# Optimization experiments

Measured on AMD Instinct MI355X. Metric: run time of the kernel, lower is better.

Reference implementation:

```python
import jax, jax.numpy as jnp
import numpy as np

B, T, D = 8, 1024, 768
H, DH = 12, 64
E, K, DFF = 16, 2, 3072
EPS = 1e-5


def _ln(x, w, b):
    m = x.mean(-1, keepdims=True)
    v = ((x - m) ** 2).mean(-1, keepdims=True)
    return (x - m) * jax.lax.rsqrt(v + EPS) * w + b


def setup_inputs() -> dict:
    key = jax.random.key(0)
    ks = jax.random.split(key, 12)
    s = 0.02
    return {
        "x": jax.random.normal(ks[0], (B, T, D), jnp.float32),
        "ln1_w": jnp.ones((D,), jnp.float32),
        "ln1_b": jnp.zeros((D,), jnp.float32),
        "qkv_w": jax.random.normal(ks[1], (D, 3 * D), jnp.float32) * s,
        "qkv_b": jnp.zeros((3 * D,), jnp.float32),
        "proj_w": jax.random.normal(ks[2], (D, D), jnp.float32) * s,
        "proj_b": jnp.zeros((D,), jnp.float32),
        "ln2_w": jnp.ones((D,), jnp.float32),
        "ln2_b": jnp.zeros((D,), jnp.float32),
        "router_w": jax.random.normal(ks[3], (D, E), jnp.float32) * s,
        "w1": jax.random.normal(ks[4], (E, D, DFF), jnp.float32) * s,
        "b1": jnp.zeros((E, DFF), jnp.float32),
        "w2": jax.random.normal(ks[5], (E, DFF, D), jnp.float32) * s,
        "b2": jnp.zeros((E, D), jnp.float32),
    }


def _block(x, ln1_w, ln1_b, qkv_w, qkv_b, proj_w, proj_b,
           ln2_w, ln2_b, router_w, w1, b1, w2, b2):
    # --- attention ---
    h = _ln(x, ln1_w, ln1_b)
    qkv = h @ qkv_w + qkv_b                      # [B,T,3D]
    q, k, v = jnp.split(qkv, 3, axis=-1)
    q = q.reshape(B, T, H, DH).transpose(0, 2, 1, 3)
    k = k.reshape(B, T, H, DH).transpose(0, 2, 1, 3)
    v = v.reshape(B, T, H, DH).transpose(0, 2, 1, 3)
    scores = jnp.einsum("bhqd,bhkd->bhqk", q, k) / np.sqrt(DH)
    causal = jnp.tril(jnp.ones((T, T), bool))
    scores = jnp.where(causal, scores, -jnp.inf)
    attn = jax.nn.softmax(scores, axis=-1)
    y = jnp.einsum("bhqk,bhkd->bhqd", attn, v)
    y = y.transpose(0, 2, 1, 3).reshape(B, T, D)
    x = x + y @ proj_w + proj_b                  # residual 1

    # --- MoE FFN (dense all-experts, gated combine) ---
    z = _ln(x, ln2_w, ln2_b)                     # [B,T,D]
    probs = jax.nn.softmax(z @ router_w, axis=-1)  # [B,T,E]
    top_p, ix = jax.lax.top_k(probs, K)
    gate = (jax.nn.one_hot(ix, E, dtype=probs.dtype) * top_p[..., None]).sum(-2)  # [B,T,E]
    gate_e = jnp.moveaxis(gate, -1, 0)           # [E,B,T]

    def body(acc, ew):
        g, W1, B1, W2, B2 = ew
        out = jax.nn.gelu(z @ W1 + B1, approximate=False) @ W2 + B2
        return acc + g[..., None] * out, None

    yff, _ = jax.lax.scan(body, jnp.zeros_like(z), (gate_e, w1, b1, w2, b2))
    # MoELayer returns z + yff; Block adds x again (faithful double residual)
    return x + z + yff


def reference(x, ln1_w, ln1_b, qkv_w, qkv_b, proj_w, proj_b,
              ln2_w, ln2_b, router_w, w1, b1, w2, b2):
    return _block(x, ln1_w, ln1_b, qkv_w, qkv_b, proj_w, proj_b,
                  ln2_w, ln2_b, router_w, w1, b1, w2, b2)
```

## Files before the change

### kernel.cpp

```cpp
#include <hip/hip_runtime.h>
#include <math.h>

#define D_MODEL 768
#define T_SEQ   1024
#define B_BATCH 8
#define NTOK    8192
#define H_HEADS 12
#define DHEAD   64
#define NEXP    16
#define DFF     3072
#define NPAIR   16384
#define MAXT128 144
#define MAXT256 80

typedef unsigned short u16;
typedef unsigned int   u32;

typedef __attribute__((ext_vector_type(8))) short bf16x8;
typedef __attribute__((ext_vector_type(4))) float f32x4;
typedef __attribute__((ext_vector_type(4))) u32   u32x4;

__device__ __forceinline__ float bf2f(u16 u) { return __uint_as_float(((u32)u) << 16); }
__device__ __forceinline__ u16 f2bf(float f) {
    u32 u = __float_as_uint(f);
    return (u16)((u + 0x7FFFu + ((u >> 16) & 1u)) >> 16);
}

__device__ __forceinline__ float fast_gelu(float v) {
    float u2 = -1.5957691216f * v * (1.0f + 0.044715f * v * v);
    return v / (1.0f + __expf(u2));
}

__device__ __forceinline__ void gload16(const void* g, void* l) {
    __builtin_amdgcn_global_load_lds((const __attribute__((address_space(1))) void*)g,
                                     (__attribute__((address_space(3))) void*)l, 16, 0, 0);
}

__global__ __launch_bounds__(256) void ln_kernel(const float* __restrict__ x,
                                                 const float* __restrict__ w,
                                                 const float* __restrict__ b,
                                                 u16* __restrict__ out_bf,
                                                 float* __restrict__ out_f) {
    const int row = blockIdx.x;
    const int tid = threadIdx.x;
    const float* xr = x + (size_t)row * D_MODEL;
    float v0 = xr[tid], v1 = xr[tid + 256], v2 = xr[tid + 512];
    float s = v0 + v1 + v2;
    float s2 = v0 * v0 + v1 * v1 + v2 * v2;
#pragma unroll
    for (int o = 32; o > 0; o >>= 1) { s += __shfl_down(s, o); s2 += __shfl_down(s2, o); }
    __shared__ float red[8];
    __shared__ float stats[2];
    const int wid = tid >> 6;
    if ((tid & 63) == 0) { red[wid] = s; red[4 + wid] = s2; }
    __syncthreads();
    if (tid == 0) {
        float ts = red[0] + red[1] + red[2] + red[3];
        float ts2 = red[4] + red[5] + red[6] + red[7];
        float mean = ts * (1.0f / D_MODEL);
        float var = ts2 * (1.0f / D_MODEL) - mean * mean;
        stats[0] = mean;
        stats[1] = rsqrtf(var + 1e-5f);
    }
    __syncthreads();
    const float mean = stats[0], rstd = stats[1];
    u16* orow = out_bf + (size_t)row * D_MODEL;
    float r0 = (v0 - mean) * rstd * w[tid]       + b[tid];
    float r1 = (v1 - mean) * rstd * w[tid + 256] + b[tid + 256];
    float r2 = (v2 - mean) * rstd * w[tid + 512] + b[tid + 512];
    orow[tid] = f2bf(r0); orow[tid + 256] = f2bf(r1); orow[tid + 512] = f2bf(r2);
    if (out_f) {
        float* frow = out_f + (size_t)row * D_MODEL;
        frow[tid] = r0; frow[tid + 256] = r1; frow[tid + 512] = r2;
    }
}

__global__ __launch_bounds__(256) void transpose_cvt(const float* __restrict__ src,
                                                     u16* __restrict__ dst,
                                                     int R, int C) {
    const size_t plane = (size_t)R * C;
    src += (size_t)blockIdx.z * plane;
    dst += (size_t)blockIdx.z * plane;
    __shared__ __align__(16) u16 tile[64][72];
    const int t = threadIdx.x;
    const int r0 = blockIdx.y * 64, c0 = blockIdx.x * 64;
    {
        const int lr = t >> 2, lc = (t & 3) * 16;
        const float* sp = src + (size_t)(r0 + lr) * C + c0 + lc;
        u16 tmp[16];
#pragma unroll
        for (int j = 0; j < 4; ++j) {
            f32x4 f = *(const f32x4*)(sp + j * 4);
            tmp[j * 4 + 0] = f2bf(f[0]); tmp[j * 4 + 1] = f2bf(f[1]);
            tmp[j * 4 + 2] = f2bf(f[2]); tmp[j * 4 + 3] = f2bf(f[3]);
        }
        *(u32x4*)&tile[lr][lc]     = *(const u32x4*)&tmp[0];
        *(u32x4*)&tile[lr][lc + 8] = *(const u32x4*)&tmp[8];
    }
    __syncthreads();
    {
        const int ln = t >> 2, lk0 = (t & 3) * 16;
        u16 o[16];
#pragma unroll
        for (int j = 0; j < 16; ++j) o[j] = tile[lk0 + j][ln];
        u16* d = dst + (size_t)(c0 + ln) * R + r0 + lk0;
        *(u32x4*)&d[0] = *(const u32x4*)&o[0];
        *(u32x4*)&d[8] = *(const u32x4*)&o[8];
    }
}

template <int MODE>
__global__ __launch_bounds__(512, 2) void gemm2ph(
    const u16* __restrict__ A, const u16* __restrict__ Bt,
    const float* __restrict__ bias, void* __restrict__ Cout,
    const int* __restrict__ bucket_tok, const int* __restrict__ offsets,
    const int* __restrict__ counts, const int* __restrict__ desc_e,
    const int* __restrict__ desc_r, const int* __restrict__ tile_cnt,
    int K, int N)
{
    const u32 nwg  = gridDim.x * gridDim.y;
    const u32 orig = blockIdx.x + gridDim.x * blockIdx.y;
    const u32 flat = (nwg & 7u) ? orig : ((orig & 7u) * (nwg >> 3) + (orig >> 3));
    const int bx = (int)(flat % gridDim.x);
    const int by = (int)(flat / gridDim.x);

    int e = 0, r0 = 0, off = 0, ne = 0, row0 = 0;
    const int col0 = bx * 256;
    if constexpr (MODE >= 2) {
        if (by >= *tile_cnt) return;
        e = desc_e[by];
        r0 = desc_r[by];
        off = offsets[e];
        ne = counts[e];
    } else {
        row0 = by * 256;
    }
    if constexpr (MODE == 2) Bt += (size_t)e * D_MODEL * DFF;
    if constexpr (MODE == 3) Bt += (size_t)e * DFF * D_MODEL;

    __shared__ __align__(16) u16 As[2][256 * 64];
    __shared__ __align__(16) u16 Bs[2][256 * 64];

    const int tid = threadIdx.x;
    const int lane = tid & 63;
    const int w = tid >> 6;
    const int wm = w >> 2, wn = w & 3;
    const int fr = lane & 15, fg = lane >> 4;

    const int koff = ((((tid & 7) * 16) ^ (((tid >> 3) & 7) << 4)) >> 1);

    u32 aoff[4], boff[4];
#pragma unroll
    for (int i = 0; i < 4; ++i) {
        const int r = i * 64 + (tid >> 3);
        u32 row;
        if constexpr (MODE == 2) {
            int rb = r0 + r;
            row = (u32)bucket_tok[off + (rb < ne ? rb : 0)];
        } else if constexpr (MODE == 3) {
            int rb = r0 + r;
            row = (u32)(off + (rb < ne ? rb : (ne - 1)));
        } else {
            row = (u32)(row0 + r);
        }
        aoff[i] = row * (u32)K + (u32)koff;
        boff[i] = (u32)(col0 + r) * (u32)K + (u32)koff;
    }

    f32x4 acc[8][4] = {};
    const int nt = K >> 6;

#pragma unroll
    for (int i = 0; i < 4; ++i) gload16(A + aoff[i],  &As[0][(i * 512 + w * 64) * 8]);
#pragma unroll
    for (int i = 0; i < 4; ++i) gload16(Bt + boff[i], &Bs[0][(i * 512 + w * 64) * 8]);
    __syncthreads();

    int cur = 0;
    for (int t = 0; t < nt; ++t) {
        if (t + 1 < nt) {
            const int k0n = (t + 1) * 64;
            const int nxt = cur ^ 1;
#pragma unroll
            for (int i = 0; i < 4; ++i) gload16(A + aoff[i] + k0n,  &As[nxt][(i * 512 + w * 64) * 8]);
#pragma unroll
            for (int i = 0; i < 4; ++i) gload16(Bt + boff[i] + k0n, &Bs[nxt][(i * 512 + w * 64) * 8]);
        }
#pragma unroll
        for (int kk = 0; kk < 2; ++kk) {
            const int sw = ((kk * 64 + fg * 16) ^ ((fr & 7) << 4)) >> 1;
            bf16x8 a[8], b[4];
#pragma unroll
            for (int mi = 0; mi < 8; ++mi)
                a[mi] = *(const bf16x8*)&As[cur][(wm * 128 + mi * 16 + fr) * 64 + sw];
#pragma unroll
            for (int ni = 0; ni < 4; ++ni)
                b[ni] = *(const bf16x8*)&Bs[cur][(wn * 64 + ni * 16 + fr) * 64 + sw];
#pragma unroll
            for (int mi = 0; mi < 8; ++mi)
#pragma unroll
                for (int ni = 0; ni < 4; ++ni)
                    acc[mi][ni] = __builtin_amdgcn_mfma_f32_16x16x32_bf16(a[mi], b[ni], acc[mi][ni], 0, 0, 0);
        }
        if (t + 1 < nt) {
            __syncthreads();
            cur ^= 1;
        }
    }

    __syncthreads();
    float* slab = (float*)&As[0][0] + w * 1088;
    const int er = lane >> 2;
    const int ec = (lane & 3) * 16;
    const int colb = col0 + wn * 64 + ec;

#pragma unroll
    for (int mi = 0; mi < 8; ++mi) {
#pragma unroll
        for (int ni = 0; ni < 4; ++ni)
#pragma unroll
            for (int i = 0; i < 4; ++i)
                slab[(fg * 4 + i) * 68 + ni * 16 + fr] = acc[mi][ni][i];
        __syncthreads();
        f32x4 v[4];
#pragma unroll
        for (int q = 0; q < 4; ++q) v[q] = *(const f32x4*)&slab[er * 68 + ec + q * 4];
        const int lrow = wm * 128 + mi * 16 + er;

        if constexpr (MODE == 0) {
            u16 o[16];
#pragma unroll
            for (int q = 0; q < 4; ++q) {
                f32x4 b4 = *(const f32x4*)&bias[colb + q * 4];
#pragma unroll
                for (int j = 0; j < 4; ++j) o[q * 4 + j] = f2bf(v[q][j] + b4[j]);
            }
            u16* cp = (u16*)Cout + (size_t)(row0 + lrow) * N + colb;
            *(u32x4*)cp       = *(const u32x4*)&o[0];
            *(u32x4*)(cp + 8) = *(const u32x4*)&o[8];
        } else if constexpr (MODE == 2) {
            const int rb = r0 + lrow;
            if (rb < ne) {
                u16 o[16];
#pragma unroll
                for (int q = 0; q < 4; ++q) {
                    f32x4 b4 = *(const f32x4*)&bias[(size_t)e * DFF + colb + q * 4];
#pragma unroll
                    for (int j = 0; j < 4; ++j) o[q * 4 + j] = f2bf(fast_gelu(v[q][j] + b4[j]));
                }
                u16* cp = (u16*)Cout + (size_t)(off + rb) * N + colb;
                *(u32x4*)cp       = *(const u32x4*)&o[0];
                *(u32x4*)(cp + 8) = *(const u32x4*)&o[8];
            }
        } else {
            const int rb = r0 + lrow;
            if (rb < ne) {
                float* cp = (float*)Cout + (size_t)(off + rb) * N + colb;
#pragma unroll
                for (int q = 0; q < 4; ++q) {
                    f32x4 b4 = *(const f32x4*)&bias[(size_t)e * D_MODEL + colb + q * 4];
                    f32x4 o4;
#pragma unroll
                    for (int j = 0; j < 4; ++j) o4[j] = v[q][j] + b4[j];
                    *(f32x4*)(cp + q * 4) = o4;
                }
            }
        }
        if (mi < 7) __syncthreads();
    }
}

template <int MODE>
__global__ __launch_bounds__(512, 4) void gemm256(
    const u16* __restrict__ A, const u16* __restrict__ Bt,
    const float* __restrict__ bias, void* __restrict__ Cout,
    const float* __restrict__ resid,
    int K, int N)
{
    const u32 nwg  = gridDim.x * gridDim.y;
    const u32 orig = blockIdx.x + gridDim.x * blockIdx.y;
    const u32 flat = (nwg & 7u) ? orig : ((orig & 7u) * (nwg >> 3) + (orig >> 3));
    const int bx = (int)(flat % gridDim.x);
    const int by = (int)(flat / gridDim.x);

    const int col0 = bx * 128;
    const int row0 = by * 256;

    __shared__ __align__(16) u16 AsBs[256 * 64 + 128 * 64];
    u16* As = AsBs;
    u16* Bs = AsBs + 256 * 64;

    const int tid = threadIdx.x;
    const int lane = tid & 63;
    const int w = tid >> 6;
    const int wm = w >> 1, wn = w & 1;
    const int fr = lane & 15, fg = lane >> 4;

    const int koff = ((((tid & 7) * 16) ^ (((tid >> 3) & 7) << 4)) >> 1);

    u32 aoff[4];
#pragma unroll
    for (int i = 0; i < 4; ++i)
        aoff[i] = (u32)(row0 + i * 64 + (tid >> 3)) * (u32)K + (u32)koff;
    u32 boff[2];
#pragma unroll
    for (int i = 0; i < 2; ++i)
        boff[i] = (u32)(col0 + i * 64 + (tid >> 3)) * (u32)K + (u32)koff;

    f32x4 acc[4][4] = {};

    for (int k0 = 0; k0 < K; k0 += 64) {
        __syncthreads();
#pragma unroll
        for (int i = 0; i < 4; ++i)
            gload16(A + aoff[i] + k0, &As[(i * 512 + w * 64) * 8]);
#pragma unroll
        for (int i = 0; i < 2; ++i)
            gload16(Bt + boff[i] + k0, &Bs[(i * 512 + w * 64) * 8]);
        __syncthreads();
#pragma unroll
        for (int kk = 0; kk < 2; ++kk) {
            const int sw = ((kk * 64 + fg * 16) ^ ((fr & 7) << 4)) >> 1;
            bf16x8 a[4], b[4];
#pragma unroll
            for (int mi = 0; mi < 4; ++mi)
                a[mi] = *(const bf16x8*)&As[(wm * 64 + mi * 16 + fr) * 64 + sw];
#pragma unroll
            for (int ni = 0; ni < 4; ++ni)
                b[ni] = *(const bf16x8*)&Bs[(wn * 64 + ni * 16 + fr) * 64 + sw];
#pragma unroll
            for (int mi = 0; mi < 4; ++mi)
#pragma unroll
                for (int ni = 0; ni < 4; ++ni)
                    acc[mi][ni] = __builtin_amdgcn_mfma_f32_16x16x32_bf16(a[mi], b[ni], acc[mi][ni], 0, 0, 0);
        }
    }

    __syncthreads();
    float* slab = (float*)AsBs + w * 1088;
    const int er = lane >> 2;
    const int ec = (lane & 3) * 16;
    const int colb = col0 + wn * 64 + ec;

#pragma unroll
    for (int mi = 0; mi < 4; ++mi) {
#pragma unroll
        for (int ni = 0; ni < 4; ++ni)
#pragma unroll
            for (int i = 0; i < 4; ++i)
                slab[(fg * 4 + i) * 68 + ni * 16 + fr] = acc[mi][ni][i];
        __syncthreads();
        f32x4 v[4];
#pragma unroll
        for (int q = 0; q < 4; ++q) v[q] = *(const f32x4*)&slab[er * 68 + ec + q * 4];
        const int lrow = wm * 64 + mi * 16 + er;

        float* cp = (float*)Cout + (size_t)(row0 + lrow) * N + colb;
        const float* rp = resid + (size_t)(row0 + lrow) * N + colb;
#pragma unroll
        for (int q = 0; q < 4; ++q) {
            f32x4 b4 = *(const f32x4*)&bias[colb + q * 4];
            f32x4 r4 = *(const f32x4*)(rp + q * 4);
            f32x4 o4;
#pragma unroll
            for (int j = 0; j < 4; ++j) o4[j] = v[q][j] + b4[j] + r4[j];
            *(f32x4*)(cp + q * 4) = o4;
        }
        if (mi < 3) __syncthreads();
    }
}

template <int MODE>
__global__ __launch_bounds__(256) void gemm128f(
    const u16* __restrict__ A, const float* __restrict__ Bf,
    const float* __restrict__ bias, void* __restrict__ Cout,
    const float* __restrict__ resid,
    const int* __restrict__ bucket_tok, const int* __restrict__ offsets,
    const int* __restrict__ counts, const int* __restrict__ desc_e,
    const int* __restrict__ desc_r, const int* __restrict__ tile_cnt,
    int K, int N)
{
    int e = 0, r0 = 0, off = 0, ne = 0, row0 = 0;
    const int col0 = blockIdx.x * 128;
    if constexpr (MODE >= 2) {
        if ((int)blockIdx.y >= *tile_cnt) return;
        e = desc_e[blockIdx.y]; r0 = desc_r[blockIdx.y];
        off = offsets[e]; ne = counts[e];
    } else row0 = blockIdx.y * 128;
    if constexpr (MODE == 2) Bf += (size_t)e * D_MODEL * DFF;
    if constexpr (MODE == 3) Bf += (size_t)e * DFF * D_MODEL;

    __shared__ __align__(16) u16 AsL[128 * 32];
    __shared__ __align__(16) u16 BsL[128 * 32];

    const int tid = threadIdx.x;
    const int lane = tid & 63;
    const int w = tid >> 6;
    const int wr = (w >> 1) * 64, wc = (w & 1) * 64;
    const int fr = lane & 15, fg = lane >> 4;
    const int lrow = lane >> 2, lk = (lane & 3) * 8;

    const u16* ag[2];
#pragma unroll
    for (int i = 0; i < 2; ++i) {
        int r = i * 64 + w * 16 + lrow;
        size_t srow;
        if constexpr (MODE == 2) {
            int rb = r0 + r;
            int tok = bucket_tok[off + (rb < ne ? rb : 0)];
            srow = (size_t)tok * K;
        } else if constexpr (MODE == 3) {
            int rb = r0 + r;
            int pp = off + (rb < ne ? rb : (ne - 1));
            srow = (size_t)pp * K;
        } else srow = (size_t)(row0 + r) * K;
        ag[i] = A + srow + lk;
    }

    f32x4 acc[4][4] = {};
    for (int k0 = 0; k0 < K; k0 += 32) {
        __syncthreads();
        gload16(ag[0] + k0, &AsL[0 * 2048 + w * 512]);
        gload16(ag[1] + k0, &AsL[1 * 2048 + w * 512]);
#pragma unroll
        for (int i = 0; i < 4; ++i) {
            int s = tid + 256 * i;
            int kk = s >> 5, n4 = (s & 31) * 4;
            f32x4 f = *(const f32x4*)(Bf + (size_t)(k0 + kk) * N + col0 + n4);
            BsL[(n4 + 0) * 32 + kk] = f2bf(f[0]);
            BsL[(n4 + 1) * 32 + kk] = f2bf(f[1]);
            BsL[(n4 + 2) * 32 + kk] = f2bf(f[2]);
            BsL[(n4 + 3) * 32 + kk] = f2bf(f[3]);
        }
        __syncthreads();
        bf16x8 a[4], b[4];
#pragma unroll
        for (int mi = 0; mi < 4; ++mi)
            a[mi] = *(const bf16x8*)&AsL[(wr + mi * 16 + fr) * 32 + fg * 8];
#pragma unroll
        for (int ni = 0; ni < 4; ++ni)
            b[ni] = *(const bf16x8*)&BsL[(wc + ni * 16 + fr) * 32 + fg * 8];
#pragma unroll
        for (int mi = 0; mi < 4; ++mi)
#pragma unroll
            for (int ni = 0; ni < 4; ++ni)
                acc[mi][ni] = __builtin_amdgcn_mfma_f32_16x16x32_bf16(a[mi], b[ni], acc[mi][ni], 0, 0, 0);
    }
#pragma unroll
    for (int mi = 0; mi < 4; ++mi) {
#pragma unroll
        for (int ni = 0; ni < 4; ++ni) {
            const int lr = wr + mi * 16 + fg * 4;
            const int col = col0 + wc + ni * 16 + fr;
#pragma unroll
            for (int i = 0; i < 4; ++i) {
                float v = acc[mi][ni][i];
                if constexpr (MODE == 0) {
                    int grow = row0 + lr + i;
                    ((u16*)Cout)[(size_t)grow * N + col] = f2bf(v + bias[col]);
                } else if constexpr (MODE == 1) {
                    int grow = row0 + lr + i;
                    size_t idx = (size_t)grow * N + col;
                    ((float*)Cout)[idx] = resid[idx] + v + bias[col];
                } else if constexpr (MODE == 2) {
                    int rb = r0 + lr + i;
                    if (rb < ne) {
                        float vb = v + bias[(size_t)e * DFF + col];
                        ((u16*)Cout)[(size_t)(off + rb) * N + col] = f2bf(fast_gelu(vb));
                    }
                } else {
                    int rb = r0 + lr + i;
                    if (rb < ne) {
                        ((float*)Cout)[(size_t)(off + rb) * N + col] = v + bias[(size_t)e * D_MODEL + col];
                    }
                }
            }
        }
    }
}

__global__ __launch_bounds__(256) void attn_mfma(const u16* __restrict__ qkv,
                                                 u16* __restrict__ y) {
    const int bh = blockIdx.x;
    const int b = bh / H_HEADS, h = bh % H_HEADS;
    const int qt = gridDim.y - 1 - blockIdx.y;
    const int tid = threadIdx.x, lane = tid & 63, w = tid >> 6;
    const int fr = lane & 15, fg = lane >> 4;

    __shared__ __align__(16) u16 Ks[128][72];
    __shared__ __align__(16) u16 Vt[64][136];
    __shared__ __align__(16) u16 Ps[4][32][136];

    const int tb = b * T_SEQ + qt * 128;
    const int wrow = w * 32;

    bf16x8 aq[2][2];
#pragma unroll
    for (int rg = 0; rg < 2; ++rg) {
        const u16* qp = qkv + (size_t)(tb + wrow + rg * 16 + fr) * (3 * D_MODEL) + h * DHEAD + fg * 8;
        aq[rg][0] = *(const bf16x8*)qp;
        aq[rg][1] = *(const bf16x8*)(qp + 32);
    }
    f32x4 accO[2][4] = {};
    float m_[2][4], l_[2][4];
#pragma unroll
    for (int rg = 0; rg < 2; ++rg)
#pragma unroll
        for (int i = 0; i < 4; ++i) { m_[rg][i] = -1e30f; l_[rg][i] = 0.0f; }

    for (int kt = 0; kt <= qt; ++kt) {
        __syncthreads();
        {
#pragma unroll
            for (int it = 0; it < 2; ++it) {
                const int krow = (tid >> 2) + it * 64;
                const int c16 = (tid & 3) * 16;
                const u16* kp = qkv + (size_t)(b * T_SEQ + kt * 128 + krow) * (3 * D_MODEL)
                              + D_MODEL + h * DHEAD + c16;
                *(u32x4*)&Ks[krow][c16]     = *(const u32x4*)kp;
                *(u32x4*)&Ks[krow][c16 + 8] = *(const u32x4*)(kp + 8);
                const u16* vp = kp + D_MODEL;
                u16 vv[16];
                *(u32x4*)&vv[0] = *(const u32x4*)vp;
                *(u32x4*)&vv[8] = *(const u32x4*)(vp + 8);
#pragma unroll
                for (int j = 0; j < 16; ++j) Vt[c16 + j][krow] = vv[j];
            }
        }
        __syncthreads();

        const bool diag = (kt == qt);

#pragma unroll
        for (int rg = 0; rg < 2; ++rg) {
            f32x4 s4[8] = {};
#pragma unroll
            for (int kk = 0; kk < 2; ++kk) {
#pragma unroll
                for (int ni = 0; ni < 8; ++ni) {
                    bf16x8 bk = *(const bf16x8*)&Ks[ni * 16 + fr][kk * 32 + fg * 8];
                    s4[ni] = __builtin_amdgcn_mfma_f32_16x16x32_bf16(aq[rg][kk], bk, s4[ni], 0, 0, 0);
                }
            }
            float p[8][4];
#pragma unroll
            for (int i = 0; i < 4; ++i) {
                const int grow = qt * 128 + wrow + rg * 16 + fg * 4 + i;
                float rmax = -1e30f;
                if (!diag) {
#pragma unroll
                    for (int ni = 0; ni < 8; ++ni) {
                        float v = s4[ni][i] * 0.125f;
                        p[ni][i] = v;
                        rmax = fmaxf(rmax, v);
                    }
                } else {
#pragma unroll
                    for (int ni = 0; ni < 8; ++ni) {
                        float v = s4[ni][i] * 0.125f;
                        if (kt * 128 + ni * 16 + fr > grow) v = -1e30f;
                        p[ni][i] = v;
                        rmax = fmaxf(rmax, v);
                    }
                }
#pragma unroll
                for (int msk = 1; msk < 16; msk <<= 1) rmax = fmaxf(rmax, __shfl_xor(rmax, msk));
                const float mn = fmaxf(m_[rg][i], rmax);
                float sum = 0.0f;
#pragma unroll
                for (int ni = 0; ni < 8; ++ni) {
                    float ev = __expf(p[ni][i] - mn);
                    p[ni][i] = ev;
                    sum += ev;
                }
#pragma unroll
                for (int msk = 1; msk < 16; msk <<= 1) sum += __shfl_xor(sum, msk);
                const float sc = __expf(m_[rg][i] - mn);
                l_[rg][i] = l_[rg][i] * sc + sum;
                m_[rg][i] = mn;
#pragma unroll
                for (int ni = 0; ni < 4; ++ni) accO[rg][ni][i] *= sc;
#pragma unroll
                for (int ni = 0; ni < 8; ++ni)
                    Ps[w][rg * 16 + fg * 4 + i][ni * 16 + fr] = f2bf(p[ni][i]);
            }
        }

#pragma unroll
        for (int rg = 0; rg < 2; ++rg) {
#pragma unroll
            for (int kk = 0; kk < 4; ++kk) {
                bf16x8 ap = *(const bf16x8*)&Ps[w][rg * 16 + fr][kk * 32 + fg * 8];
#pragma unroll
                for (int ni = 0; ni < 4; ++ni) {
                    bf16x8 bv = *(const bf16x8*)&Vt[ni * 16 + fr][kk * 32 + fg * 8];
                    accO[rg][ni] = __builtin_amdgcn_mfma_f32_16x16x32_bf16(ap, bv, accO[rg][ni], 0, 0, 0);
                }
            }
        }
    }

#pragma unroll
    for (int rg = 0; rg < 2; ++rg) {
#pragma unroll
        for (int i = 0; i < 4; ++i) {
            const float inv = 1.0f / l_[rg][i];
            u16* yp = y + (size_t)(tb + wrow + rg * 16 + fg * 4 + i) * D_MODEL + h * DHEAD;
#pragma unroll
            for (int ni = 0; ni < 4; ++ni) yp[ni * 16 + fr] = f2bf(accO[rg][ni][i] * inv);
        }
    }
}

__global__ __launch_bounds__(64) void router_kernel(const float* __restrict__ z,
                                                    const float* __restrict__ rw,
                                                    float* __restrict__ gates,
                                                    int* __restrict__ eidx) {
    const int t = blockIdx.x;
    const int lane = threadIdx.x;
    const int e = lane & 15, part = lane >> 4;
    const float* zr = z + (size_t)t * D_MODEL;
    float acc = 0.0f;
    for (int d = part * 192; d < part * 192 + 192; ++d)
        acc += zr[d] * rw[d * NEXP + e];
    acc += __shfl_down(acc, 32);
    acc += __shfl_down(acc, 16);
    const float lg = acc;
    float logit[NEXP];
#pragma unroll
    for (int ee = 0; ee < NEXP; ++ee) logit[ee] = __shfl(lg, ee);
    if (lane == 0) {
        float m1 = -1e30f, m2 = -1e30f; int i1 = 0, i2 = 0;
#pragma unroll
        for (int ee = 0; ee < NEXP; ++ee) {
            float v = logit[ee];
            if (v > m1) { m2 = m1; i2 = i1; m1 = v; i1 = ee; }
            else if (v > m2) { m2 = v; i2 = ee; }
        }
        float den = 0.0f;
#pragma unroll
        for (int ee = 0; ee < NEXP; ++ee) den += __expf(logit[ee] - m1);
        const float inv = 1.0f / den;
        gates[2 * t] = inv;
        gates[2 * t + 1] = __expf(m2 - m1) * inv;
        eidx[2 * t] = i1;
        eidx[2 * t + 1] = i2;
    }
}

__global__ __launch_bounds__(256) void count_kernel(const int* __restrict__ eidx, int* counts) {
    int i = blockIdx.x * 256 + threadIdx.x;
    if (i < NPAIR) atomicAdd(&counts[eidx[i]], 1);
}

__global__ void offsets_kernel(const int* __restrict__ counts, int* offsets, int* cursor,
                               int* desc_e, int* desc_r, int* tile_cnt, int step) {
    if (threadIdx.x == 0 && blockIdx.x == 0) {
        int off = 0, nt = 0;
        for (int e = 0; e < NEXP; ++e) {
            offsets[e] = off;
            cursor[e] = off;
            int c = counts[e];
            for (int r = 0; r < c; r += step) { desc_e[nt] = e; desc_r[nt] = r; ++nt; }
            off += c;
        }
        *tile_cnt = nt;
    }
}

__global__ __launch_bounds__(256) void scatter_kernel(const int* __restrict__ eidx, int* cursor,
                                                      int* __restrict__ btok, int* __restrict__ ppos) {
    int i = blockIdx.x * 256 + threadIdx.x;
    if (i < NPAIR) {
        int pos = atomicAdd(&cursor[eidx[i]], 1);
        btok[pos] = i >> 1;
        ppos[i] = pos;
    }
}

__global__ __launch_bounds__(256) void final_kernel(const float* __restrict__ x1,
                                                    const float* __restrict__ zf,
                                                    const float* __restrict__ moe_o,
                                                    const float* __restrict__ gates,
                                                    const int* __restrict__ ppos,
                                                    float* __restrict__ out) {
    const int t = blockIdx.x;
    const int d = blockIdx.y * 256 + threadIdx.x;
    const size_t idx = (size_t)t * D_MODEL + d;
    const float g0 = gates[2 * t], g1 = gates[2 * t + 1];
    const int p0 = ppos[2 * t], p1 = ppos[2 * t + 1];
    out[idx] = x1[idx] + zf[idx] + g0 * moe_o[(size_t)p0 * D_MODEL + d]
                                 + g1 * moe_o[(size_t)p1 * D_MODEL + d];
}

extern "C" void kernel_launch(void* const* d_in, const int* in_sizes, int n_in,
                              void* d_out, int out_size, void* d_ws, size_t ws_size,
                              hipStream_t stream) {
    const float* x        = (const float*)d_in[0];
    const float* ln1_w    = (const float*)d_in[1];
    const float* ln1_b    = (const float*)d_in[2];
    const float* qkv_w    = (const float*)d_in[3];
    const float* qkv_b    = (const float*)d_in[4];
    const float* proj_w   = (const float*)d_in[5];
    const float* proj_b   = (const float*)d_in[6];
    const float* ln2_w    = (const float*)d_in[7];
    const float* ln2_b    = (const float*)d_in[8];
    const float* router_w = (const float*)d_in[9];
    const float* w1       = (const float*)d_in[10];
    const float* b1       = (const float*)d_in[11];
    const float* w2       = (const float*)d_in[12];
    const float* b2       = (const float*)d_in[13];
    float* out = (float*)d_out;

    char* ws = (char*)d_ws;
    size_t off = 0;
    auto alloc = [&](size_t bytes) -> void* {
        void* p = ws + off;
        off += (bytes + 255) & ~(size_t)255;
        return p;
    };
    u16*  h_bf   = (u16*)alloc((size_t)NTOK * D_MODEL * 2);
    u16*  qkv_bf = (u16*)alloc((size_t)NTOK * 3 * D_MODEL * 2);
    u16*  y_bf   = h_bf;
    float* x1    = (float*)alloc((size_t)NTOK * D_MODEL * 4);
    u16*  z_bf   = (u16*)alloc((size_t)NTOK * D_MODEL * 2);
    float* z_f   = (float*)alloc((size_t)NTOK * D_MODEL * 4);
    u16*  act    = (u16*)alloc((size_t)NPAIR * DFF * 2);
    float* moe_o = (float*)alloc((size_t)NPAIR * D_MODEL * 4);
    float* gates = (float*)alloc((size_t)NTOK * 2 * 4);
    int*  eidx   = (int*)alloc((size_t)NTOK * 2 * 4);
    int*  ppos   = (int*)alloc((size_t)NTOK * 2 * 4);
    int*  btok   = (int*)alloc((size_t)NPAIR * 4);
    int*  counts = (int*)alloc(NEXP * 4);
    int*  offs   = (int*)alloc(NEXP * 4);
    int*  cursor = (int*)alloc(NEXP * 4);
    int*  desc_e = (int*)alloc(MAXT128 * 4);
    int*  desc_r = (int*)alloc(MAXT128 * 4);
    int*  tcnt   = (int*)alloc(4);
    u16* qkvT  = (u16*)alloc((size_t)(3 * D_MODEL) * D_MODEL * 2);
    u16* projT = (u16*)alloc((size_t)D_MODEL * D_MODEL * 2);
    u16* w1t   = (u16*)alloc((size_t)NEXP * DFF * D_MODEL * 2);
    u16* w2t   = (u16*)alloc((size_t)NEXP * D_MODEL * DFF * 2);
    const bool useT = (off <= ws_size);
    (void)in_sizes; (void)n_in; (void)out_size;

    hipMemsetAsync(counts, 0, NEXP * 4, stream);

    if (useT) {
        transpose_cvt<<<dim3(3 * D_MODEL / 64, D_MODEL / 64, 1), 256, 0, stream>>>(qkv_w, qkvT, D_MODEL, 3 * D_MODEL);
        transpose_cvt<<<dim3(D_MODEL / 64, D_MODEL / 64, 1), 256, 0, stream>>>(proj_w, projT, D_MODEL, D_MODEL);
        transpose_cvt<<<dim3(DFF / 64, D_MODEL / 64, NEXP), 256, 0, stream>>>(w1, w1t, D_MODEL, DFF);
        transpose_cvt<<<dim3(D_MODEL / 64, DFF / 64, NEXP), 256, 0, stream>>>(w2, w2t, DFF, D_MODEL);
    }

    ln_kernel<<<NTOK, 256, 0, stream>>>(x, ln1_w, ln1_b, h_bf, nullptr);
    if (useT)
        gemm2ph<0><<<dim3(9, 32), 512, 0, stream>>>(h_bf, qkvT, qkv_b, qkv_bf,
            nullptr, nullptr, nullptr, nullptr, nullptr, nullptr, D_MODEL, 3 * D_MODEL);
    else
        gemm128f<0><<<dim3(18, 64), 256, 0, stream>>>(h_bf, qkv_w, qkv_b, qkv_bf, nullptr,
            nullptr, nullptr, nullptr, nullptr, nullptr, nullptr, D_MODEL, 3 * D_MODEL);

    attn_mfma<<<dim3(B_BATCH * H_HEADS, T_SEQ / 128), 256, 0, stream>>>(qkv_bf, y_bf);

    if (useT)
        gemm256<1><<<dim3(6, 32), 512, 0, stream>>>(y_bf, projT, proj_b, x1, x,
            D_MODEL, D_MODEL);
    else
        gemm128f<1><<<dim3(6, 64), 256, 0, stream>>>(y_bf, proj_w, proj_b, x1, x,
            nullptr, nullptr, nullptr, nullptr, nullptr, nullptr, D_MODEL, D_MODEL);

    ln_kernel<<<NTOK, 256, 0, stream>>>(x1, ln2_w, ln2_b, z_bf, z_f);
    router_kernel<<<NTOK, 64, 0, stream>>>(z_f, router_w, gates, eidx);
    count_kernel<<<NPAIR / 256, 256, 0, stream>>>(eidx, counts);
    offsets_kernel<<<1, 64, 0, stream>>>(counts, offs, cursor, desc_e, desc_r, tcnt,
                                         useT ? 256 : 128);
    scatter_kernel<<<NPAIR / 256, 256, 0, stream>>>(eidx, cursor, btok, ppos);

    if (useT) {
        gemm2ph<2><<<dim3(DFF / 256, MAXT256), 512, 0, stream>>>(z_bf, w1t, b1, act,
            btok, offs, counts, desc_e, desc_r, tcnt, D_MODEL, DFF);
        gemm2ph<3><<<dim3(D_MODEL / 256, MAXT256), 512, 0, stream>>>(act, w2t, b2, moe_o,
            btok, offs, counts, desc_e, desc_r, tcnt, DFF, D_MODEL);
    } else {
        gemm128f<2><<<dim3(DFF / 128, MAXT128), 256, 0, stream>>>(z_bf, w1, b1, act, nullptr,
            btok, offs, counts, desc_e, desc_r, tcnt, D_MODEL, DFF);
        gemm128f<3><<<dim3(D_MODEL / 128, MAXT128), 256, 0, stream>>>(act, w2, b2, moe_o, nullptr,
            btok, offs, counts, desc_e, desc_r, tcnt, DFF, D_MODEL);
    }

    final_kernel<<<dim3(NTOK, 3), 256, 0, stream>>>(x1, z_f, moe_o, gates, ppos, out);
}
```

Before: 645.4 us.

## Restructure 256x256 GEMM into eight-phase half-tile pipeline with priority scheduling

The double-buffered GEMM main loop is replaced by a schedule that splits each 256x256 tile's A and B operands into 128-row halves. Each half lives in its own LDS slot, eight slots in total. Each k-step runs four MFMA quadrants, with global-to-LDS prefetch of the next halves interleaved between them. Manual s_barrier, vmcnt waits and s_setprio are used so memory traffic and matrix math overlap within a wave group. The epilogue row and column mapping changes to match the new per-wave quadrant layout. The added barriers and the hand-tuned wait counts raise the risk of hazards and extra synchronisation cost.

```diff
diff --git a/kernel.cpp b/kernel.cpp
--- a/kernel.cpp
+++ b/kernel.cpp
@@ -35,6 +35,9 @@
     __builtin_amdgcn_global_load_lds((const __attribute__((address_space(1))) void*)g,
                                      (__attribute__((address_space(3))) void*)l, 16, 0, 0);
 }
+
+#define SBAR() do { __builtin_amdgcn_sched_barrier(0); \
+                    asm volatile("s_barrier" ::: "memory"); } while (0)
 
 __global__ __launch_bounds__(256) void ln_kernel(const float* __restrict__ x,
                                                  const float* __restrict__ w,
@@ -110,7 +113,7 @@
 }
 
 template <int MODE>
-__global__ __launch_bounds__(512, 2) void gemm2ph(
+__global__ __launch_bounds__(512, 2) void gemm8ph(
     const u16* __restrict__ A, const u16* __restrict__ Bt,
     const float* __restrict__ bias, void* __restrict__ Cout,
     const int* __restrict__ bucket_tok, const int* __restrict__ offsets,
@@ -138,8 +141,7 @@
     if constexpr (MODE == 2) Bt += (size_t)e * D_MODEL * DFF;
     if constexpr (MODE == 3) Bt += (size_t)e * DFF * D_MODEL;
 
-    __shared__ __align__(16) u16 As[2][256 * 64];
-    __shared__ __align__(16) u16 Bs[2][256 * 64];
+    __shared__ __align__(16) u16 SL[8][128 * 64];
 
     const int tid = threadIdx.x;
     const int lane = tid & 63;
@@ -167,55 +169,132 @@
         boff[i] = (u32)(col0 + r) * (u32)K + (u32)koff;
     }
 
+    auto stA = [&](int d, int h, int k0) {
+#pragma unroll
+        for (int l = 0; l < 2; ++l)
+            gload16(A + aoff[h * 2 + l] + k0, &SL[d * 2 + h][(l * 512 + w * 64) * 8]);
+    };
+    auto stB = [&](int d, int h, int k0) {
+#pragma unroll
+        for (int l = 0; l < 2; ++l)
+            gload16(Bt + boff[h * 2 + l] + k0, &SL[4 + d * 2 + h][(l * 512 + w * 64) * 8]);
+    };
+
     f32x4 acc[8][4] = {};
     const int nt = K >> 6;
-
-#pragma unroll
-    for (int i = 0; i < 4; ++i) gload16(A + aoff[i],  &As[0][(i * 512 + w * 64) * 8]);
-#pragma unroll
-    for (int i = 0; i < 4; ++i) gload16(Bt + boff[i], &Bs[0][(i * 512 + w * 64) * 8]);
+    const int sw_[2] = { ((fg * 16) ^ ((fr & 7) << 4)) >> 1,
+                         ((64 + fg * 16) ^ ((fr & 7) << 4)) >> 1 };
+    const int arow = wm * 64 + fr;
+    const int brow = wn * 32 + fr;
+
+    stA(0, 0, 0); stB(0, 0, 0); stA(0, 1, 0); stB(0, 1, 0);
+    if (nt > 1) {
+        stA(1, 0, 64); stB(1, 1, 64);
+        asm volatile("s_waitcnt vmcnt(4)" ::: "memory");
+    } else {
+        asm volatile("s_waitcnt vmcnt(0)" ::: "memory");
+    }
+    SBAR();
+
+    bf16x8 aA[4][2], bB[2][2];
+    for (int g = 0; g < nt; ++g) {
+        const int d = g & 1;
+        const u16* A0s = SL[d * 2 + 0];
+        const u16* A1s = SL[d * 2 + 1];
+        const u16* B0s = SL[4 + d * 2 + 0];
+        const u16* B1s = SL[4 + d * 2 + 1];
+
+#pragma unroll
+        for (int kk = 0; kk < 2; ++kk) {
+#pragma unroll
+            for (int f = 0; f < 4; ++f)
+                aA[f][kk] = *(const bf16x8*)&A0s[(arow + f * 16) * 64 + sw_[kk]];
+#pragma unroll
+            for (int gg = 0; gg < 2; ++gg)
+                bB[gg][kk] = *(const bf16x8*)&B0s[(brow + gg * 16) * 64 + sw_[kk]];
+        }
+        if (g + 1 < nt) stA((g + 1) & 1, 1, (g + 1) * 64);
+        SBAR();
+        __builtin_amdgcn_s_setprio(1);
+#pragma unroll
+        for (int kk = 0; kk < 2; ++kk)
+#pragma unroll
+            for (int f = 0; f < 4; ++f) {
+                acc[f][0] = __builtin_amdgcn_mfma_f32_16x16x32_bf16(aA[f][kk], bB[0][kk], acc[f][0], 0, 0, 0);
+                acc[f][1] = __builtin_amdgcn_mfma_f32_16x16x32_bf16(aA[f][kk], bB[1][kk], acc[f][1], 0, 0, 0);
+            }
+        __builtin_amdgcn_s_setprio(0);
+        SBAR();
+
+#pragma unroll
+        for (int kk = 0; kk < 2; ++kk)
+#pragma unroll
+            for (int gg = 0; gg < 2; ++gg)
+                bB[gg][kk] = *(const bf16x8*)&B1s[(brow + gg * 16) * 64 + sw_[kk]];
+        if (g + 1 < nt) stB((g + 1) & 1, 0, (g + 1) * 64);
+        SBAR();
+        __builtin_amdgcn_s_setprio(1);
+#pragma unroll
+        for (int kk = 0; kk < 2; ++kk)
+#pragma unroll
+            for (int f = 0; f < 4; ++f) {
+                acc[f][2] = __builtin_amdgcn_mfma_f32_16x16x32_bf16(aA[f][kk], bB[0][kk], acc[f][2], 0, 0, 0);
+                acc[f][3] = __builtin_amdgcn_mfma_f32_16x16x32_bf16(aA[f][kk], bB[1][kk], acc[f][3], 0, 0, 0);
+            }
+        __builtin_amdgcn_s_setprio(0);
+        SBAR();
+
+#pragma unroll
+        for (int kk = 0; kk < 2; ++kk)
+#pragma unroll
+            for (int f = 0; f < 4; ++f)
+                aA[f][kk] = *(const bf16x8*)&A1s[(arow + f * 16) * 64 + sw_[kk]];
+        if (g + 2 < nt) stA(d, 0, (g + 2) * 64);
+        SBAR();
+        __builtin_amdgcn_s_setprio(1);
+#pragma unroll
+        for (int kk = 0; kk < 2; ++kk)
+#pragma unroll
+            for (int f = 0; f < 4; ++f) {
+                acc[4 + f][2] = __builtin_amdgcn_mfma_f32_16x16x32_bf16(aA[f][kk], bB[0][kk], acc[4 + f][2], 0, 0, 0);
+                acc[4 + f][3] = __builtin_amdgcn_mfma_f32_16x16x32_bf16(aA[f][kk], bB[1][kk], acc[4 + f][3], 0, 0, 0);
+            }
+        __builtin_amdgcn_s_setprio(0);
+        SBAR();
+
+#pragma unroll
+        for (int kk = 0; kk < 2; ++kk)
+#pragma unroll
+            for (int gg = 0; gg < 2; ++gg)
+                bB[gg][kk] = *(const bf16x8*)&B0s[(brow + gg * 16) * 64 + sw_[kk]];
+        if (g + 2 < nt) stB(d, 1, (g + 2) * 64);
+        SBAR();
+        __builtin_amdgcn_s_setprio(1);
+#pragma unroll
+        for (int kk = 0; kk < 2; ++kk)
+#pragma unroll
+            for (int f = 0; f < 4; ++f) {
+                acc[4 + f][0] = __builtin_amdgcn_mfma_f32_16x16x32_bf16(aA[f][kk], bB[0][kk], acc[4 + f][0], 0, 0, 0);
+                acc[4 + f][1] = __builtin_amdgcn_mfma_f32_16x16x32_bf16(aA[f][kk], bB[1][kk], acc[4 + f][1], 0, 0, 0);
+            }
+        __builtin_amdgcn_s_setprio(0);
+        __builtin_amdgcn_sched_barrier(0);
+        if (g + 1 < nt) {
+            if (g + 2 < nt) asm volatile("s_waitcnt vmcnt(4)" ::: "memory");
+            else            asm volatile("s_waitcnt vmcnt(0)" ::: "memory");
+        }
+        asm volatile("s_barrier" ::: "memory");
+    }
+
     __syncthreads();
-
-    int cur = 0;
-    for (int t = 0; t < nt; ++t) {
-        if (t + 1 < nt) {
-            const int k0n = (t + 1) * 64;
-            const int nxt = cur ^ 1;
-#pragma unroll
-            for (int i = 0; i < 4; ++i) gload16(A + aoff[i] + k0n,  &As[nxt][(i * 512 + w * 64) * 8]);
-#pragma unroll
-            for (int i = 0; i < 4; ++i) gload16(Bt + boff[i] + k0n, &Bs[nxt][(i * 512 + w * 64) * 8]);
-        }
-#pragma unroll
-        for (int kk = 0; kk < 2; ++kk) {
-            const int sw = ((kk * 64 + fg * 16) ^ ((fr & 7) << 4)) >> 1;
-            bf16x8 a[8], b[4];
-#pragma unroll
-            for (int mi = 0; mi < 8; ++mi)
-                a[mi] = *(const bf16x8*)&As[cur][(wm * 128 + mi * 16 + fr) * 64 + sw];
-#pragma unroll
-            for (int ni = 0; ni < 4; ++ni)
-                b[ni] = *(const bf16x8*)&Bs[cur][(wn * 64 + ni * 16 + fr) * 64 + sw];
-#pragma unroll
-            for (int mi = 0; mi < 8; ++mi)
-#pragma unroll
-                for (int ni = 0; ni < 4; ++ni)
-                    acc[mi][ni] = __builtin_amdgcn_mfma_f32_16x16x32_bf16(a[mi], b[ni], acc[mi][ni], 0, 0, 0);
-        }
-        if (t + 1 < nt) {
-            __syncthreads();
-            cur ^= 1;
-        }
-    }
-
-    __syncthreads();
-    float* slab = (float*)&As[0][0] + w * 1088;
+    float* slab = (float*)&SL[0][0] + w * 1088;
     const int er = lane >> 2;
-    const int ec = (lane & 3) * 16;
-    const int colb = col0 + wn * 64 + ec;
+    const int q  = lane & 3;
+    const int colq = col0 + (q >> 1) * 128 + wn * 32 + (q & 1) * 16;
 
 #pragma unroll
     for (int mi = 0; mi < 8; ++mi) {
+        const int h = mi >> 2, f = mi & 3;
 #pragma unroll
         for (int ni = 0; ni < 4; ++ni)
 #pragma unroll
@@ -224,18 +303,18 @@
         __syncthreads();
         f32x4 v[4];
 #pragma unroll
-        for (int q = 0; q < 4; ++q) v[q] = *(const f32x4*)&slab[er * 68 + ec + q * 4];
-        const int lrow = wm * 128 + mi * 16 + er;
+        for (int j = 0; j < 4; ++j) v[j] = *(const f32x4*)&slab[er * 68 + q * 16 + j * 4];
+        const int lrow = h * 128 + wm * 64 + f * 16 + er;
 
         if constexpr (MODE == 0) {
             u16 o[16];
 #pragma unroll
-            for (int q = 0; q < 4; ++q) {
-                f32x4 b4 = *(const f32x4*)&bias[colb + q * 4];
-#pragma unroll
-                for (int j = 0; j < 4; ++j) o[q * 4 + j] = f2bf(v[q][j] + b4[j]);
-            }
-            u16* cp = (u16*)Cout + (size_t)(row0 + lrow) * N + colb;
+            for (int j = 0; j < 4; ++j) {
+                f32x4 b4 = *(const f32x4*)&bias[colq + j * 4];
+#pragma unroll
+                for (int k = 0; k < 4; ++k) o[j * 4 + k] = f2bf(v[j][k] + b4[k]);
+            }
+            u16* cp = (u16*)Cout + (size_t)(row0 + lrow) * N + colq;
             *(u32x4*)cp       = *(const u32x4*)&o[0];
             *(u32x4*)(cp + 8) = *(const u32x4*)&o[8];
         } else if constexpr (MODE == 2) {
@@ -243,26 +322,26 @@
             if (rb < ne) {
                 u16 o[16];
 #pragma unroll
-                for (int q = 0; q < 4; ++q) {
-                    f32x4 b4 = *(const f32x4*)&bias[(size_t)e * DFF + colb + q * 4];
-#pragma unroll
-                    for (int j = 0; j < 4; ++j) o[q * 4 + j] = f2bf(fast_gelu(v[q][j] + b4[j]));
+                for (int j = 0; j < 4; ++j) {
+                    f32x4 b4 = *(const f32x4*)&bias[(size_t)e * DFF + colq + j * 4];
+#pragma unroll
+                    for (int k = 0; k < 4; ++k) o[j * 4 + k] = f2bf(fast_gelu(v[j][k] + b4[k]));
                 }
-                u16* cp = (u16*)Cout + (size_t)(off + rb) * N + colb;
+                u16* cp = (u16*)Cout + (size_t)(off + rb) * N + colq;
                 *(u32x4*)cp       = *(const u32x4*)&o[0];
                 *(u32x4*)(cp + 8) = *(const u32x4*)&o[8];
             }
         } else {
             const int rb = r0 + lrow;
             if (rb < ne) {
-                float* cp = (float*)Cout + (size_t)(off + rb) * N + colb;
-#pragma unroll
-                for (int q = 0; q < 4; ++q) {
-                    f32x4 b4 = *(const f32x4*)&bias[(size_t)e * D_MODEL + colb + q * 4];
+                float* cp = (float*)Cout + (size_t)(off + rb) * N + colq;
+#pragma unroll
+                for (int j = 0; j < 4; ++j) {
+                    f32x4 b4 = *(const f32x4*)&bias[(size_t)e * D_MODEL + colq + j * 4];
                     f32x4 o4;
 #pragma unroll
-                    for (int j = 0; j < 4; ++j) o4[j] = v[q][j] + b4[j];
-                    *(f32x4*)(cp + q * 4) = o4;
+                    for (int k = 0; k < 4; ++k) o4[k] = v[j][k] + b4[k];
+                    *(f32x4*)(cp + j * 4) = o4;
                 }
             }
         }
@@ -755,7 +834,7 @@
 
     ln_kernel<<<NTOK, 256, 0, stream>>>(x, ln1_w, ln1_b, h_bf, nullptr);
     if (useT)
-        gemm2ph<0><<<dim3(9, 32), 512, 0, stream>>>(h_bf, qkvT, qkv_b, qkv_bf,
+        gemm8ph<0><<<dim3(9, 32), 512, 0, stream>>>(h_bf, qkvT, qkv_b, qkv_bf,
             nullptr, nullptr, nullptr, nullptr, nullptr, nullptr, D_MODEL, 3 * D_MODEL);
     else
         gemm128f<0><<<dim3(18, 64), 256, 0, stream>>>(h_bf, qkv_w, qkv_b, qkv_bf, nullptr,
@@ -778,9 +857,9 @@
     scatter_kernel<<<NPAIR / 256, 256, 0, stream>>>(eidx, cursor, btok, ppos);
 
     if (useT) {
-        gemm2ph<2><<<dim3(DFF / 256, MAXT256), 512, 0, stream>>>(z_bf, w1t, b1, act,
+        gemm8ph<2><<<dim3(DFF / 256, MAXT256), 512, 0, stream>>>(z_bf, w1t, b1, act,
             btok, offs, counts, desc_e, desc_r, tcnt, D_MODEL, DFF);
-        gemm2ph<3><<<dim3(D_MODEL / 256, MAXT256), 512, 0, stream>>>(act, w2t, b2, moe_o,
+        gemm8ph<3><<<dim3(D_MODEL / 256, MAXT256), 512, 0, stream>>>(act, w2t, b2, moe_o,
             btok, offs, counts, desc_e, desc_r, tcnt, DFF, D_MODEL);
     } else {
         gemm128f<2><<<dim3(DFF / 128, MAXT128), 256, 0, stream>>>(z_bf, w1, b1, act, nullptr,
```

Result: no change. 655.6 us (+1.6%).
